# Performance work log

Measured on AMD Instinct MI355X. Metric: run time of the kernel, lower is better.

Reference implementation:

```python
import jax, jax.numpy as jnp
import numpy as np

B, T, E, H = 4, 1024, 1024, 16
F = E // H  # head_feature = 64
EPS = 1e-5


def setup_inputs() -> dict:
    key = jax.random.key(0)
    ks = jax.random.split(key, 7)
    return {
        "x": jax.random.normal(ks[0], (B, T, E), dtype=jnp.float32),
        "q_w": jax.random.normal(ks[1], (H, E, F), dtype=jnp.float32),
        "k_w": jax.random.normal(ks[2], (H, E, F), dtype=jnp.float32),
        "v_w": jax.random.normal(ks[3], (H, E, F), dtype=jnp.float32),
        "fr_w": jax.random.normal(ks[4], (B, E, E), dtype=jnp.float32),
        "ff_w": jax.random.normal(ks[5], (E, E), dtype=jnp.float32),
        "ff_b": jax.random.normal(ks[6], (E,), dtype=jnp.float32),
        "ln1_w": jnp.ones((T, E), dtype=jnp.float32),
        "ln1_b": jnp.zeros((T, E), dtype=jnp.float32),
        "ln2_w": jnp.ones((T, E), dtype=jnp.float32),
        "ln2_b": jnp.zeros((T, E), dtype=jnp.float32),
    }


def _layernorm_2d(x, w, b):
    # LayerNorm over the last TWO dims ([T, E]), matching nn.LayerNorm([T, E])
    mean = jnp.mean(x, axis=(-2, -1), keepdims=True)
    var = jnp.mean(jnp.square(x - mean), axis=(-2, -1), keepdims=True)
    return (x - mean) * jax.lax.rsqrt(var + EPS) * w + b


def _attention(x, q_w, k_w, v_w, fr_w):
    # projections: [B,T,E] x [H,E,F] -> [B,H,T,F]
    q = jnp.einsum("bte,hef->bhtf", x, q_w)
    k = jnp.einsum("bte,hef->bhtf", x, k_w)
    v = jnp.einsum("bte,hef->bhtf", x, v_w)
    scores = jnp.einsum("bhqf,bhkf->bhqk", q, k)  # [B,H,T,T]
    # faithful to source: multiplicative mask (-1e9 on strict upper tri, +1 added everywhere)
    ones = jnp.ones((T, T), dtype=scores.dtype)
    mask = -1.0e9 * jnp.triu(ones, k=1) + ones
    scores = scores * mask
    attn = jax.nn.softmax(scores / jnp.sqrt(jnp.float32(F)), axis=-1)
    z = jnp.einsum("bhqk,bhkf->bhqf", attn, v)  # [B,H,T,F]
    z = z.transpose(0, 2, 1, 3).reshape(B, T, E)  # merge heads
    return jnp.einsum("bte,bed->btd", z, fr_w)  # per-batch feature reduction


def reference(x, q_w, k_w, v_w, fr_w, ff_w, ff_b, ln1_w, ln1_b, ln2_w, ln2_b):
    z = _attention(x, q_w, k_w, v_w, fr_w)
    z1 = _layernorm_2d(x + z, ln1_w, ln1_b)
    z2 = jax.nn.relu(jnp.einsum("bte,de->btd", z1, ff_w) + ff_b)
    return _layernorm_2d(z1 + z2, ln2_w, ln2_b)
```

## Files before the change

kernel.cpp:

```cpp
#include <hip/hip_runtime.h>
#include <math.h>

constexpr int Bc = 4, Tc = 1024, Ec = 1024, Hc = 16, Fc = 64;

typedef __attribute__((ext_vector_type(8))) short bf16x8;
typedef __attribute__((ext_vector_type(4))) float f32x4;

__device__ __forceinline__ ushort f2bf(float x) {
  union { float f; unsigned u; } v; v.f = x;
  unsigned r = v.u + 0x7fffu + ((v.u >> 16) & 1u);
  return (ushort)(r >> 16);
}
__device__ __forceinline__ float bf2f(ushort h) {
  union { float f; unsigned u; } v; v.u = ((unsigned)h) << 16; return v.f;
}
__device__ __forceinline__ void split3(float x, ushort& h, ushort& m, ushort& l) {
  h = f2bf(x);
  float r1 = x - bf2f(h);
  m = f2bf(r1);
  float r2 = r1 - bf2f(m);
  l = f2bf(r2);
}
__device__ __forceinline__ void split2(float x, ushort& h, ushort& l) {
  h = f2bf(x);
  l = f2bf(x - bf2f(h));
}

__global__ __launch_bounds__(256) void transp_w(
    const float* __restrict__ qw, const float* __restrict__ kw,
    const float* __restrict__ vw, ushort* __restrict__ wT)
{
  const int zi = blockIdx.z;
  const float* src = (zi == 0) ? qw : (zi == 1) ? kw : vw;
  ushort* dst = wT + (size_t)(zi * 3) * (1u << 20);
  const int ns = (zi == 2) ? 1 : 3;
  const int h = blockIdx.y, e0 = blockIdx.x * 64;
  __shared__ float T[64][68];
  const int tid = threadIdx.x;
  {
    const int er = tid >> 4, fr = (tid & 15) * 4;
#pragma unroll
    for (int i = 0; i < 4; ++i) {
      const float4 v = *(const float4*)&src[((size_t)(h * 1024 + e0 + er + i * 16)) * 64 + fr];
      *(float4*)&T[er + i * 16][fr] = v;
    }
  }
  __syncthreads();
  const int f = tid >> 2, eo = (tid & 3) * 16;
  ushort hs[16], ms[16], ls[16];
#pragma unroll
  for (int j = 0; j < 16; ++j) {
    split3(T[eo + j][f], hs[j], ms[j], ls[j]);
  }
  const size_t nbase = (size_t)(h * 64 + f) * 1024 + e0 + eo;
  bf16x8 v0, v1;
#pragma unroll
  for (int j = 0; j < 8; ++j) { v0[j] = (short)hs[j]; v1[j] = (short)hs[j + 8]; }
  *(bf16x8*)&dst[nbase] = v0; *(bf16x8*)&dst[nbase + 8] = v1;
  if (ns == 3) {
#pragma unroll
    for (int j = 0; j < 8; ++j) { v0[j] = (short)ms[j]; v1[j] = (short)ms[j + 8]; }
    *(bf16x8*)&dst[(1u << 20) + nbase] = v0; *(bf16x8*)&dst[(1u << 20) + nbase + 8] = v1;
#pragma unroll
    for (int j = 0; j < 8; ++j) { v0[j] = (short)ls[j]; v1[j] = (short)ls[j + 8]; }
    *(bf16x8*)&dst[(2u << 20) + nbase] = v0; *(bf16x8*)&dst[(2u << 20) + nbase + 8] = v1;
  }
}

__global__ __launch_bounds__(256) void transp_frw(
    const float* __restrict__ frw, ushort* __restrict__ frT)
{
  const int bb = blockIdx.z;
  const int e0 = blockIdx.x * 64, d0 = blockIdx.y * 64;
  __shared__ float T[64][68];
  const int tid = threadIdx.x;
  {
    const int er = tid >> 4, dr = (tid & 15) * 4;
#pragma unroll
    for (int i = 0; i < 4; ++i) {
      const float4 v = *(const float4*)&frw[((size_t)bb * 1024 + e0 + er + i * 16) * 1024 + d0 + dr];
      *(float4*)&T[er + i * 16][dr] = v;
    }
  }
  __syncthreads();
  const int d = tid >> 2, eo = (tid & 3) * 16;
  ushort hs[16], ls[16];
#pragma unroll
  for (int j = 0; j < 16; ++j) split2(T[eo + j][d], hs[j], ls[j]);
  const size_t nbase = ((size_t)bb * 1024 + d0 + d) * 1024 + e0 + eo;
  bf16x8 v0, v1;
#pragma unroll
  for (int j = 0; j < 8; ++j) { v0[j] = (short)hs[j]; v1[j] = (short)hs[j + 8]; }
  *(bf16x8*)&frT[nbase] = v0; *(bf16x8*)&frT[nbase + 8] = v1;
#pragma unroll
  for (int j = 0; j < 8; ++j) { v0[j] = (short)ls[j]; v1[j] = (short)ls[j + 8]; }
  *(bf16x8*)&frT[(4u << 20) + nbase] = v0; *(bf16x8*)&frT[(4u << 20) + nbase + 8] = v1;
}

__global__ __launch_bounds__(256) void proj_qk_mfma(
    const float* __restrict__ x, const ushort* __restrict__ wT,
    float* __restrict__ qf, ushort* __restrict__ kh,
    ushort* __restrict__ km, ushort* __restrict__ kl)
{
  const int zi = blockIdx.z;
  const ushort* wt = wT + (size_t)zi * 3 * (1u << 20);
  const int m0 = blockIdx.x * 128, n0 = blockIdx.y * 128;
  __shared__ ushort As[3][128][36];
  __shared__ ushort Bs[3][128][36];
  const int tid = threadIdx.x;
  const int wave = tid >> 6, lane = tid & 63, l15 = lane & 15, quad = lane >> 4;
  const int wm = wave >> 1, wn = wave & 1;
  const int sr = tid >> 1, sk = (tid & 1) * 16;
  f32x4 acc[4][4] = {};
  for (int k0 = 0; k0 < 1024; k0 += 32) {
    __syncthreads();
    {
      const float* ap = x + (size_t)(m0 + sr) * 1024 + k0 + sk;
      float xs[16];
      *(float4*)&xs[0]  = *(const float4*)(ap);
      *(float4*)&xs[4]  = *(const float4*)(ap + 4);
      *(float4*)&xs[8]  = *(const float4*)(ap + 8);
      *(float4*)&xs[12] = *(const float4*)(ap + 12);
      bf16x8 h0, h1, m0v, m1v, l0, l1;
#pragma unroll
      for (int j = 0; j < 8; ++j) {
        ushort hu, mu, lu;
        split3(xs[j], hu, mu, lu);
        h0[j] = (short)hu; m0v[j] = (short)mu; l0[j] = (short)lu;
        split3(xs[j + 8], hu, mu, lu);
        h1[j] = (short)hu; m1v[j] = (short)mu; l1[j] = (short)lu;
      }
      *(bf16x8*)&As[0][sr][sk] = h0;  *(bf16x8*)&As[0][sr][sk + 8] = h1;
      *(bf16x8*)&As[1][sr][sk] = m0v; *(bf16x8*)&As[1][sr][sk + 8] = m1v;
      *(bf16x8*)&As[2][sr][sk] = l0;  *(bf16x8*)&As[2][sr][sk + 8] = l1;
#pragma unroll
      for (int s = 0; s < 3; ++s) {
        const ushort* bp = wt + ((size_t)s << 20) + (size_t)(n0 + sr) * 1024 + k0 + sk;
        *(bf16x8*)&Bs[s][sr][sk]     = *(const bf16x8*)(bp);
        *(bf16x8*)&Bs[s][sr][sk + 8] = *(const bf16x8*)(bp + 8);
      }
    }
    __syncthreads();
    bf16x8 af[4][3];
#pragma unroll
    for (int tm = 0; tm < 4; ++tm)
#pragma unroll
      for (int s = 0; s < 3; ++s)
        af[tm][s] = *(const bf16x8*)&As[s][wm * 64 + tm * 16 + l15][quad * 8];
#pragma unroll
    for (int tn = 0; tn < 4; ++tn) {
      const int nrow = wn * 64 + tn * 16 + l15;
      bf16x8 b0 = *(const bf16x8*)&Bs[0][nrow][quad * 8];
      bf16x8 b1 = *(const bf16x8*)&Bs[1][nrow][quad * 8];
      bf16x8 b2 = *(const bf16x8*)&Bs[2][nrow][quad * 8];
#pragma unroll
      for (int tm = 0; tm < 4; ++tm) {
        f32x4 a = acc[tm][tn];
        a = __builtin_amdgcn_mfma_f32_16x16x32_bf16(af[tm][0], b0, a, 0, 0, 0);
        a = __builtin_amdgcn_mfma_f32_16x16x32_bf16(af[tm][0], b1, a, 0, 0, 0);
        a = __builtin_amdgcn_mfma_f32_16x16x32_bf16(af[tm][1], b0, a, 0, 0, 0);
        a = __builtin_amdgcn_mfma_f32_16x16x32_bf16(af[tm][0], b2, a, 0, 0, 0);
        a = __builtin_amdgcn_mfma_f32_16x16x32_bf16(af[tm][1], b1, a, 0, 0, 0);
        a = __builtin_amdgcn_mfma_f32_16x16x32_bf16(af[tm][2], b0, a, 0, 0, 0);
        acc[tm][tn] = a;
      }
    }
  }
#pragma unroll
  for (int tm = 0; tm < 4; ++tm) {
#pragma unroll
    for (int tn = 0; tn < 4; ++tn) {
#pragma unroll
      for (int r = 0; r < 4; ++r) {
        int m = m0 + wm * 64 + tm * 16 + quad * 4 + r;
        int n = n0 + wn * 64 + tn * 16 + l15;
        int b = m >> 10, t = m & 1023, h = n >> 6, f = n & 63;
        size_t idx = (((size_t)(b * 16 + h)) * 1024 + t) * 64 + f;
        if (zi == 0) {
          qf[idx] = acc[tm][tn][r];
        } else {
          ushort hu, mu, lu;
          split3(acc[tm][tn][r], hu, mu, lu);
          kh[idx] = hu; km[idx] = mu; kl[idx] = lu;
        }
      }
    }
  }
}

__global__ __launch_bounds__(256) void proj_v_mfma(
    const float* __restrict__ x, const ushort* __restrict__ wT,
    ushort* __restrict__ vt)
{
  const ushort* wt = wT + (size_t)6 * (1u << 20);
  const int m0 = blockIdx.x * 128, n0 = blockIdx.y * 128;
  __shared__ ushort As[128][36];
  __shared__ ushort Bs[128][36];
  const int tid = threadIdx.x;
  const int wave = tid >> 6, lane = tid & 63, l15 = lane & 15, quad = lane >> 4;
  const int wm = wave >> 1, wn = wave & 1;
  const int sr = tid >> 1, sk = (tid & 1) * 16;
  f32x4 acc[4][4] = {};
  for (int k0 = 0; k0 < 1024; k0 += 32) {
    __syncthreads();
    {
      const float* ap = x + (size_t)(m0 + sr) * 1024 + k0 + sk;
      float xs[16];
      *(float4*)&xs[0]  = *(const float4*)(ap);
      *(float4*)&xs[4]  = *(const float4*)(ap + 4);
      *(float4*)&xs[8]  = *(const float4*)(ap + 8);
      *(float4*)&xs[12] = *(const float4*)(ap + 12);
      bf16x8 h0, h1;
#pragma unroll
      for (int j = 0; j < 8; ++j) {
        h0[j] = (short)f2bf(xs[j]);
        h1[j] = (short)f2bf(xs[j + 8]);
      }
      *(bf16x8*)&As[sr][sk] = h0; *(bf16x8*)&As[sr][sk + 8] = h1;
      const ushort* bp = wt + (size_t)(n0 + sr) * 1024 + k0 + sk;
      *(bf16x8*)&Bs[sr][sk]     = *(const bf16x8*)(bp);
      *(bf16x8*)&Bs[sr][sk + 8] = *(const bf16x8*)(bp + 8);
    }
    __syncthreads();
    bf16x8 af[4];
#pragma unroll
    for (int tm = 0; tm < 4; ++tm)
      af[tm] = *(const bf16x8*)&As[wm * 64 + tm * 16 + l15][quad * 8];
#pragma unroll
    for (int tn = 0; tn < 4; ++tn) {
      bf16x8 b0 = *(const bf16x8*)&Bs[wn * 64 + tn * 16 + l15][quad * 8];
#pragma unroll
      for (int tm = 0; tm < 4; ++tm)
        acc[tm][tn] = __builtin_amdgcn_mfma_f32_16x16x32_bf16(af[tm], b0, acc[tm][tn], 0, 0, 0);
    }
  }
#pragma unroll
  for (int tm = 0; tm < 4; ++tm) {
#pragma unroll
    for (int tn = 0; tn < 4; ++tn) {
#pragma unroll
      for (int r = 0; r < 4; ++r) {
        int m = m0 + wm * 64 + tm * 16 + quad * 4 + r;
        int n = n0 + wn * 64 + tn * 16 + l15;
        int b = m >> 10, t = m & 1023, h = n >> 6, f = n & 63;
        vt[(((size_t)(b * 16 + h)) * 64 + f) * 1024 + t] = f2bf(acc[tm][tn][r]);
      }
    }
  }
}

__global__ __launch_bounds__(512) void attn_mfma(
    const float* __restrict__ qf, const ushort* __restrict__ kh,
    const ushort* __restrict__ km, const ushort* __restrict__ kl,
    const ushort* __restrict__ vt, float* __restrict__ z)
{
  __shared__ ushort Ks[3][64][68];
  __shared__ ushort Vs[64][68];
  __shared__ ushort Pl[8][16][68];

  const int tid = threadIdx.x;
  const int wave = tid >> 6, lane = tid & 63;
  const int l15 = lane & 15, quad = lane >> 4;
  const int bh = blockIdx.y;
  const int qbase = blockIdx.x * 128;

  bf16x8 aqh[2], aqm[2], aql[2];
  {
    const int qrow = qbase + wave * 16 + l15;
    const float* qp = qf + ((size_t)bh * Tc + qrow) * Fc;
#pragma unroll
    for (int ks = 0; ks < 2; ++ks) {
      int f0 = ks * 32 + quad * 8;
      float4 x0 = *(const float4*)(qp + f0);
      float4 x1 = *(const float4*)(qp + f0 + 4);
      float xs[8] = {x0.x, x0.y, x0.z, x0.w, x1.x, x1.y, x1.z, x1.w};
#pragma unroll
      for (int j = 0; j < 8; ++j) {
        ushort hu, mu, lu;
        split3(xs[j], hu, mu, lu);
        aqh[ks][j] = (short)hu; aqm[ks][j] = (short)mu; aql[ks][j] = (short)lu;
      }
    }
  }

  f32x4 o[4] = {{0,0,0,0},{0,0,0,0},{0,0,0,0},{0,0,0,0}};
  float m_run[4], l_run[4];
#pragma unroll
  for (int r = 0; r < 4; ++r) { m_run[r] = -1e30f; l_run[r] = 0.f; }

  const int srow = tid >> 3, sc8 = tid & 7;
  const size_t kbase = (size_t)bh * Tc * Fc;
  const size_t vbase = (size_t)bh * Fc * Tc;
  const ushort* kp0 = kh + kbase + (size_t)srow * Fc + sc8 * 8;
  const ushort* kp1 = km + kbase + (size_t)srow * Fc + sc8 * 8;
  const ushort* kp2 = kl + kbase + (size_t)srow * Fc + sc8 * 8;
  const ushort* vp  = vt + vbase + (size_t)srow * Tc + sc8 * 8;

  for (int kt = 0; kt < Tc; kt += 64) {
    __syncthreads();
    {
      const size_t ko = (size_t)kt * Fc;
      *(bf16x8*)&Ks[0][srow][sc8 * 8] = *(const bf16x8*)(kp0 + ko);
      *(bf16x8*)&Ks[1][srow][sc8 * 8] = *(const bf16x8*)(kp1 + ko);
      *(bf16x8*)&Ks[2][srow][sc8 * 8] = *(const bf16x8*)(kp2 + ko);
      *(bf16x8*)&Vs[srow][sc8 * 8]    = *(const bf16x8*)(vp + kt);
    }
    __syncthreads();

    f32x4 sacc[4] = {{0,0,0,0},{0,0,0,0},{0,0,0,0},{0,0,0,0}};
#pragma unroll
    for (int nt = 0; nt < 4; ++nt) {
      int key = nt * 16 + l15;
#pragma unroll
      for (int ks = 0; ks < 2; ++ks) {
        int f0 = ks * 32 + quad * 8;
        bf16x8 bh_ = *(const bf16x8*)&Ks[0][key][f0];
        bf16x8 bm_ = *(const bf16x8*)&Ks[1][key][f0];
        bf16x8 bl_ = *(const bf16x8*)&Ks[2][key][f0];
        sacc[nt] = __builtin_amdgcn_mfma_f32_16x16x32_bf16(aqh[ks], bh_, sacc[nt], 0, 0, 0);
        sacc[nt] = __builtin_amdgcn_mfma_f32_16x16x32_bf16(aqh[ks], bm_, sacc[nt], 0, 0, 0);
        sacc[nt] = __builtin_amdgcn_mfma_f32_16x16x32_bf16(aqm[ks], bh_, sacc[nt], 0, 0, 0);
        sacc[nt] = __builtin_amdgcn_mfma_f32_16x16x32_bf16(aqh[ks], bl_, sacc[nt], 0, 0, 0);
        sacc[nt] = __builtin_amdgcn_mfma_f32_16x16x32_bf16(aqm[ks], bm_, sacc[nt], 0, 0, 0);
        sacc[nt] = __builtin_amdgcn_mfma_f32_16x16x32_bf16(aql[ks], bh_, sacc[nt], 0, 0, 0);
      }
    }

    const int rowg0 = qbase + wave * 16 + quad * 4;
    float mx[4];
#pragma unroll
    for (int r = 0; r < 4; ++r) mx[r] = -1e30f;
#pragma unroll
    for (int nt = 0; nt < 4; ++nt) {
      int key = kt + nt * 16 + l15;
#pragma unroll
      for (int r = 0; r < 4; ++r) {
        float s = sacc[nt][r];
        if (key > rowg0 + r) s *= -1.0e9f + 1.0f;
        s *= 0.125f;
        sacc[nt][r] = s;
        mx[r] = fmaxf(mx[r], s);
      }
    }
#pragma unroll
    for (int r = 0; r < 4; ++r)
#pragma unroll
      for (int d = 1; d < 16; d <<= 1) mx[r] = fmaxf(mx[r], __shfl_xor(mx[r], d));

    float corr[4], ps[4];
#pragma unroll
    for (int r = 0; r < 4; ++r) {
      float m2 = fmaxf(m_run[r], mx[r]);
      corr[r] = __expf(m_run[r] - m2);
      m_run[r] = m2;
      ps[r] = 0.f;
    }
#pragma unroll
    for (int nt = 0; nt < 4; ++nt) {
#pragma unroll
      for (int r = 0; r < 4; ++r) {
        float p = __expf(sacc[nt][r] - m_run[r]);
        ps[r] += p;
        Pl[wave][quad * 4 + r][nt * 16 + l15] = f2bf(p);
      }
    }
#pragma unroll
    for (int r = 0; r < 4; ++r) {
#pragma unroll
      for (int d = 1; d < 16; d <<= 1) ps[r] += __shfl_xor(ps[r], d);
      l_run[r] = l_run[r] * corr[r] + ps[r];
#pragma unroll
      for (int ft = 0; ft < 4; ++ft) o[ft][r] *= corr[r];
    }

#pragma unroll
    for (int ks2 = 0; ks2 < 2; ++ks2) {
      bf16x8 pa = *(const bf16x8*)&Pl[wave][l15][ks2 * 32 + quad * 8];
#pragma unroll
      for (int ft = 0; ft < 4; ++ft) {
        bf16x8 vb = *(const bf16x8*)&Vs[ft * 16 + l15][ks2 * 32 + quad * 8];
        o[ft] = __builtin_amdgcn_mfma_f32_16x16x32_bf16(pa, vb, o[ft], 0, 0, 0);
      }
    }
  }

  const int b = bh >> 4, h = bh & 15;
#pragma unroll
  for (int r = 0; r < 4; ++r) {
    float inv = 1.f / l_run[r];
    int row = qbase + wave * 16 + quad * 4 + r;
    float* zp = z + ((size_t)(b * Tc + row)) * Ec + h * Fc;
#pragma unroll
    for (int ft = 0; ft < 4; ++ft) zp[ft * 16 + l15] = o[ft][r] * inv;
  }
}

__global__ __launch_bounds__(256) void gemm_fr_mfma(
    const float* __restrict__ z, const ushort* __restrict__ frT,
    const float* __restrict__ x, float* __restrict__ s1,
    float2* __restrict__ part)
{
  const int bb = blockIdx.z;
  const int m0 = blockIdx.x * 128, n0 = blockIdx.y * 128;
  __shared__ ushort Ah[128][36], Al[128][36];
  __shared__ ushort Bh[128][36], Bl[128][36];
  __shared__ float2 red[256];
  const int tid = threadIdx.x;
  const int wave = tid >> 6, lane = tid & 63, l15 = lane & 15, quad = lane >> 4;
  const int wm = wave >> 1, wn = wave & 1;
  const int sr = tid >> 1, sk = (tid & 1) * 16;
  f32x4 acc[4][4] = {};
  const ushort* bhp = frT + ((size_t)bb * 1024 + n0) * 1024;
  const ushort* blp = bhp + (4u << 20);
  for (int k0 = 0; k0 < 1024; k0 += 32) {
    __syncthreads();
    {
      const float* ap = z + ((size_t)bb * 1024 + m0 + sr) * 1024 + k0 + sk;
      float xs[16];
      *(float4*)&xs[0]  = *(const float4*)(ap);
      *(float4*)&xs[4]  = *(const float4*)(ap + 4);
      *(float4*)&xs[8]  = *(const float4*)(ap + 8);
      *(float4*)&xs[12] = *(const float4*)(ap + 12);
      bf16x8 h0, h1, l0, l1;
#pragma unroll
      for (int j = 0; j < 8; ++j) {
        ushort hu, lu;
        split2(xs[j], hu, lu);     h0[j] = (short)hu; l0[j] = (short)lu;
        split2(xs[j + 8], hu, lu); h1[j] = (short)hu; l1[j] = (short)lu;
      }
      *(bf16x8*)&Ah[sr][sk] = h0; *(bf16x8*)&Ah[sr][sk + 8] = h1;
      *(bf16x8*)&Al[sr][sk] = l0; *(bf16x8*)&Al[sr][sk + 8] = l1;
      const size_t boff = (size_t)sr * 1024 + k0 + sk;
      *(bf16x8*)&Bh[sr][sk]     = *(const bf16x8*)(bhp + boff);
      *(bf16x8*)&Bh[sr][sk + 8] = *(const bf16x8*)(bhp + boff + 8);
      *(bf16x8*)&Bl[sr][sk]     = *(const bf16x8*)(blp + boff);
      *(bf16x8*)&Bl[sr][sk + 8] = *(const bf16x8*)(blp + boff + 8);
    }
    __syncthreads();
    bf16x8 ah[4], al[4];
#pragma unroll
    for (int tm = 0; tm < 4; ++tm) {
      ah[tm] = *(const bf16x8*)&Ah[wm * 64 + tm * 16 + l15][quad * 8];
      al[tm] = *(const bf16x8*)&Al[wm * 64 + tm * 16 + l15][quad * 8];
    }
#pragma unroll
    for (int tn = 0; tn < 4; ++tn) {
      const int nrow = wn * 64 + tn * 16 + l15;
      bf16x8 b0 = *(const bf16x8*)&Bh[nrow][quad * 8];
      bf16x8 b1 = *(const bf16x8*)&Bl[nrow][quad * 8];
#pragma unroll
      for (int tm = 0; tm < 4; ++tm) {
        f32x4 a = acc[tm][tn];
        a = __builtin_amdgcn_mfma_f32_16x16x32_bf16(ah[tm], b0, a, 0, 0, 0);
        a = __builtin_amdgcn_mfma_f32_16x16x32_bf16(ah[tm], b1, a, 0, 0, 0);
        a = __builtin_amdgcn_mfma_f32_16x16x32_bf16(al[tm], b0, a, 0, 0, 0);
        acc[tm][tn] = a;
      }
    }
  }
  float sum = 0.f, sq = 0.f;
#pragma unroll
  for (int tm = 0; tm < 4; ++tm) {
#pragma unroll
    for (int tn = 0; tn < 4; ++tn) {
#pragma unroll
      for (int r = 0; r < 4; ++r) {
        int m = m0 + wm * 64 + tm * 16 + quad * 4 + r;
        int n = n0 + wn * 64 + tn * 16 + l15;
        size_t idx = ((size_t)bb * 1024 + m) * 1024 + n;
        float o = x[idx] + acc[tm][tn][r];
        s1[idx] = o;
        sum += o; sq += o * o;
      }
    }
  }
  red[tid] = make_float2(sum, sq);
  __syncthreads();
  for (int s = 128; s > 0; s >>= 1) {
    if (tid < s) { red[tid].x += red[tid + s].x; red[tid].y += red[tid + s].y; }
    __syncthreads();
  }
  if (tid == 0) part[(bb * 8 + blockIdx.x) * 8 + blockIdx.y] = red[0];
}

__global__ __launch_bounds__(256) void gemm_ff_mfma(
    const float* __restrict__ z1, const float* __restrict__ ffw,
    const float* __restrict__ ffb, float* __restrict__ s2,
    float2* __restrict__ part)
{
  const int m0 = blockIdx.x * 128, n0 = blockIdx.y * 128;
  __shared__ ushort Ah[128][36], Al[128][36];
  __shared__ ushort Bh[128][36], Bl[128][36];
  __shared__ float2 red[256];
  const int tid = threadIdx.x;
  const int wave = tid >> 6, lane = tid & 63, l15 = lane & 15, quad = lane >> 4;
  const int wm = wave >> 1, wn = wave & 1;
  const int sr = tid >> 1, sk = (tid & 1) * 16;
  f32x4 acc[4][4] = {};
  for (int k0 = 0; k0 < 1024; k0 += 32) {
    __syncthreads();
    {
      const float* ap = z1 + (size_t)(m0 + sr) * 1024 + k0 + sk;
      const float* bp = ffw + (size_t)(n0 + sr) * 1024 + k0 + sk;
      float xs[16], ys[16];
      *(float4*)&xs[0]  = *(const float4*)(ap);
      *(float4*)&xs[4]  = *(const float4*)(ap + 4);
      *(float4*)&xs[8]  = *(const float4*)(ap + 8);
      *(float4*)&xs[12] = *(const float4*)(ap + 12);
      *(float4*)&ys[0]  = *(const float4*)(bp);
      *(float4*)&ys[4]  = *(const float4*)(bp + 4);
      *(float4*)&ys[8]  = *(const float4*)(bp + 8);
      *(float4*)&ys[12] = *(const float4*)(bp + 12);
      bf16x8 h0, h1, l0, l1, g0, g1, e0, e1;
#pragma unroll
      for (int j = 0; j < 8; ++j) {
        ushort hu, lu;
        split2(xs[j], hu, lu);     h0[j] = (short)hu; l0[j] = (short)lu;
        split2(xs[j + 8], hu, lu); h1[j] = (short)hu; l1[j] = (short)lu;
        split2(ys[j], hu, lu);     g0[j] = (short)hu; e0[j] = (short)lu;
        split2(ys[j + 8], hu, lu); g1[j] = (short)hu; e1[j] = (short)lu;
      }
      *(bf16x8*)&Ah[sr][sk] = h0; *(bf16x8*)&Ah[sr][sk + 8] = h1;
      *(bf16x8*)&Al[sr][sk] = l0; *(bf16x8*)&Al[sr][sk + 8] = l1;
      *(bf16x8*)&Bh[sr][sk] = g0; *(bf16x8*)&Bh[sr][sk + 8] = g1;
      *(bf16x8*)&Bl[sr][sk] = e0; *(bf16x8*)&Bl[sr][sk + 8] = e1;
    }
    __syncthreads();
    bf16x8 ah[4], al[4];
#pragma unroll
    for (int tm = 0; tm < 4; ++tm) {
      ah[tm] = *(const bf16x8*)&Ah[wm * 64 + tm * 16 + l15][quad * 8];
      al[tm] = *(const bf16x8*)&Al[wm * 64 + tm * 16 + l15][quad * 8];
    }
#pragma unroll
    for (int tn = 0; tn < 4; ++tn) {
      const int nrow = wn * 64 + tn * 16 + l15;
      bf16x8 b0 = *(const bf16x8*)&Bh[nrow][quad * 8];
      bf16x8 b1 = *(const bf16x8*)&Bl[nrow][quad * 8];
#pragma unroll
      for (int tm = 0; tm < 4; ++tm) {
        f32x4 a = acc[tm][tn];
        a = __builtin_amdgcn_mfma_f32_16x16x32_bf16(ah[tm], b0, a, 0, 0, 0);
        a = __builtin_amdgcn_mfma_f32_16x16x32_bf16(ah[tm], b1, a, 0, 0, 0);
        a = __builtin_amdgcn_mfma_f32_16x16x32_bf16(al[tm], b0, a, 0, 0, 0);
        acc[tm][tn] = a;
      }
    }
  }
  float sum = 0.f, sq = 0.f;
#pragma unroll
  for (int tm = 0; tm < 4; ++tm) {
#pragma unroll
    for (int tn = 0; tn < 4; ++tn) {
#pragma unroll
      for (int r = 0; r < 4; ++r) {
        int m = m0 + wm * 64 + tm * 16 + quad * 4 + r;
        int n = n0 + wn * 64 + tn * 16 + l15;
        size_t idx = (size_t)m * 1024 + n;
        float o = z1[idx] + fmaxf(acc[tm][tn][r] + ffb[n], 0.f);
        s2[idx] = o;
        sum += o; sq += o * o;
      }
    }
  }
  red[tid] = make_float2(sum, sq);
  __syncthreads();
  for (int s = 128; s > 0; s >>= 1) {
    if (tid < s) { red[tid].x += red[tid + s].x; red[tid].y += red[tid + s].y; }
    __syncthreads();
  }
  if (tid == 0) part[blockIdx.x * 8 + blockIdx.y] = red[0];
}

__global__ __launch_bounds__(256) void ln_stats(
    const float2* __restrict__ part, float2* __restrict__ stats, int npart)
{
  __shared__ double sd[256], sq[256];
  const int tid = threadIdx.x;
  float2 p = (tid < npart) ? part[blockIdx.x * npart + tid] : make_float2(0.f, 0.f);
  sd[tid] = (double)p.x; sq[tid] = (double)p.y;
  __syncthreads();
  for (int s = 128; s > 0; s >>= 1) {
    if (tid < s) { sd[tid] += sd[tid + s]; sq[tid] += sq[tid + s]; }
    __syncthreads();
  }
  if (tid == 0) {
    const double n = (double)Tc * Ec;
    double mean = sd[0] / n;
    double var = sq[0] / n - mean * mean;
    if (var < 0.0) var = 0.0;
    double rs = 1.0 / sqrt(var + 1e-5);
    stats[blockIdx.x] = make_float2((float)mean, (float)rs);
  }
}

__global__ __launch_bounds__(256) void ln_norm(
    const float* __restrict__ s, const float2* __restrict__ stats,
    const float* __restrict__ w, const float* __restrict__ bias,
    float* __restrict__ out)
{
  int i = blockIdx.x * 256 + threadIdx.x;
  if (i >= (Bc * Tc * Ec) / 4) return;
  int b = i >> 18;
  int te4 = i & ((1 << 18) - 1);
  float2 st = stats[b];
  float4 sv = ((const float4*)s)[i];
  float4 wv = ((const float4*)w)[te4];
  float4 bv = ((const float4*)bias)[te4];
  float4 o;
  o.x = (sv.x - st.x) * st.y * wv.x + bv.x;
  o.y = (sv.y - st.x) * st.y * wv.y + bv.y;
  o.z = (sv.z - st.x) * st.y * wv.z + bv.z;
  o.w = (sv.w - st.x) * st.y * wv.w + bv.w;
  ((float4*)out)[i] = o;
}

extern "C" void kernel_launch(void* const* d_in, const int* in_sizes, int n_in,
                              void* d_out, int out_size, void* d_ws, size_t ws_size,
                              hipStream_t stream)
{
  const float* x    = (const float*)d_in[0];
  const float* qw   = (const float*)d_in[1];
  const float* kw   = (const float*)d_in[2];
  const float* vw   = (const float*)d_in[3];
  const float* frw  = (const float*)d_in[4];
  const float* ffw  = (const float*)d_in[5];
  const float* ffb  = (const float*)d_in[6];
  const float* ln1w = (const float*)d_in[7];
  const float* ln1b = (const float*)d_in[8];
  const float* ln2w = (const float*)d_in[9];
  const float* ln2b = (const float*)d_in[10];
  float* out = (float*)d_out;
  char* W = (char*)d_ws;

  const size_t MB = 1ull << 20;
  float*  qf  = (float*)(W);
  ushort* kh  = (ushort*)(W + 16 * MB);
  ushort* km  = (ushort*)(W + 24 * MB);
  ushort* kl  = (ushort*)(W + 32 * MB);
  ushort* vt  = (ushort*)(W + 40 * MB);
  ushort* wT  = (ushort*)(W + 48 * MB);
  float*  zb  = (float*)(W + 48 * MB);
  ushort* frT = (ushort*)(W + 16 * MB);
  float*  s1  = (float*)(W);
  float*  z1  = (float*)(W + 16 * MB);
  float*  s2  = (float*)(W + 32 * MB);
  float2* part1  = (float2*)(W + 64 * MB);
  float2* part2  = part1 + 1024;
  float2* stats1 = part2 + 1024;
  float2* stats2 = stats1 + 4;

  transp_w<<<dim3(16, 16, 3), 256, 0, stream>>>(qw, kw, vw, wT);
  proj_qk_mfma<<<dim3(32, 8, 2), 256, 0, stream>>>(x, wT, qf, kh, km, kl);
  proj_v_mfma<<<dim3(32, 8), 256, 0, stream>>>(x, wT, vt);
  attn_mfma<<<dim3(8, 64), 512, 0, stream>>>(qf, kh, km, kl, vt, zb);
  transp_frw<<<dim3(16, 16, 4), 256, 0, stream>>>(frw, frT);
  gemm_fr_mfma<<<dim3(8, 8, 4), 256, 0, stream>>>(zb, frT, x, s1, part1);
  ln_stats<<<dim3(4), 256, 0, stream>>>(part1, stats1, 64);
  ln_norm<<<dim3(4096), 256, 0, stream>>>(s1, stats1, ln1w, ln1b, z1);
  gemm_ff_mfma<<<dim3(32, 8), 256, 0, stream>>>(z1, ffw, ffb, s2, part2);
  ln_stats<<<dim3(4), 256, 0, stream>>>(part2, stats2, 64);
  ln_norm<<<dim3(4096), 256, 0, stream>>>(s2, stats2, ln2w, ln2b, out);
}
```

Baseline: 480.7 us.

## Pre-split GEMM operands to bf16 and use fragment-ordered LDS layout

Moves the fp32-to-bf16 hi/lo splitting out of the GEMM inner loops. The attention epilogue, layernorm-1 and a new split_ffw kernel now emit split bf16 buffers, so gemm_fr and gemm_ff only copy bf16 tiles into LDS. The LDS tiles are reorganized into an MFMA-fragment-contiguous layout without padding to avoid bank conflicts. The QK projection switches to a truncating 3-way split, which changes rounding but keeps the residual exact. This adds an extra kernel launch and keeps padding-free LDS strides, which may create conflicts on the store side.

```diff
diff --git a/kernel.cpp b/kernel.cpp
--- a/kernel.cpp
+++ b/kernel.cpp
@@ -25,6 +25,20 @@
   h = f2bf(x);
   l = f2bf(x - bf2f(h));
 }
+__device__ __forceinline__ void split3t(float x, ushort& h, ushort& m, ushort& l) {
+  union { float f; unsigned u; } v; v.f = x;
+  h = (ushort)(v.u >> 16);
+  union { float f; unsigned u; } hf; hf.u = v.u & 0xffff0000u;
+  float r1 = x - hf.f;
+  union { float f; unsigned u; } v1; v1.f = r1;
+  m = (ushort)(v1.u >> 16);
+  union { float f; unsigned u; } mf; mf.u = v1.u & 0xffff0000u;
+  float r2 = r1 - mf.f;
+  union { float f; unsigned u; } v2; v2.f = r2;
+  l = (ushort)(v2.u >> 16);
+}
+
+#define FRAG_IDX(tile, quad, l) (((((tile) * 4) + (quad)) * 16 + (l)) * 8)
 
 __global__ __launch_bounds__(256) void transp_w(
     const float* __restrict__ qw, const float* __restrict__ kw,
@@ -49,9 +63,7 @@
   const int f = tid >> 2, eo = (tid & 3) * 16;
   ushort hs[16], ms[16], ls[16];
 #pragma unroll
-  for (int j = 0; j < 16; ++j) {
-    split3(T[eo + j][f], hs[j], ms[j], ls[j]);
-  }
+  for (int j = 0; j < 16; ++j) split3(T[eo + j][f], hs[j], ms[j], ls[j]);
   const size_t nbase = (size_t)(h * 64 + f) * 1024 + e0 + eo;
   bf16x8 v0, v1;
 #pragma unroll
@@ -97,6 +109,17 @@
   *(bf16x8*)&frT[(4u << 20) + nbase] = v0; *(bf16x8*)&frT[(4u << 20) + nbase + 8] = v1;
 }
 
+__global__ __launch_bounds__(256) void split_ffw(
+    const float* __restrict__ ffw, ushort* __restrict__ fh, ushort* __restrict__ fl)
+{
+  int i = blockIdx.x * 256 + threadIdx.x;
+  float4 v = ((const float4*)ffw)[i];
+  ushort4 h, l;
+  split2(v.x, h.x, l.x); split2(v.y, h.y, l.y);
+  split2(v.z, h.z, l.z); split2(v.w, h.w, l.w);
+  ((ushort4*)fh)[i] = h; ((ushort4*)fl)[i] = l;
+}
+
 __global__ __launch_bounds__(256) void proj_qk_mfma(
     const float* __restrict__ x, const ushort* __restrict__ wT,
     float* __restrict__ qf, ushort* __restrict__ kh,
@@ -105,17 +128,19 @@
   const int zi = blockIdx.z;
   const ushort* wt = wT + (size_t)zi * 3 * (1u << 20);
   const int m0 = blockIdx.x * 128, n0 = blockIdx.y * 128;
-  __shared__ ushort As[3][128][36];
-  __shared__ ushort Bs[3][128][36];
+  __shared__ ushort As[3 * 4096];
+  __shared__ ushort Bs[3 * 4096];
   const int tid = threadIdx.x;
   const int wave = tid >> 6, lane = tid & 63, l15 = lane & 15, quad = lane >> 4;
   const int wm = wave >> 1, wn = wave & 1;
-  const int sr = tid >> 1, sk = (tid & 1) * 16;
+  const int sr = tid >> 1, q0 = (tid & 1) * 2;
+  const int wb0 = FRAG_IDX(sr >> 4, q0, sr & 15);
+  const int wb1 = FRAG_IDX(sr >> 4, q0 + 1, sr & 15);
   f32x4 acc[4][4] = {};
   for (int k0 = 0; k0 < 1024; k0 += 32) {
     __syncthreads();
     {
-      const float* ap = x + (size_t)(m0 + sr) * 1024 + k0 + sk;
+      const float* ap = x + (size_t)(m0 + sr) * 1024 + k0 + q0 * 8;
       float xs[16];
       *(float4*)&xs[0]  = *(const float4*)(ap);
       *(float4*)&xs[4]  = *(const float4*)(ap + 4);
@@ -125,19 +150,19 @@
 #pragma unroll
       for (int j = 0; j < 8; ++j) {
         ushort hu, mu, lu;
-        split3(xs[j], hu, mu, lu);
+        split3t(xs[j], hu, mu, lu);
         h0[j] = (short)hu; m0v[j] = (short)mu; l0[j] = (short)lu;
-        split3(xs[j + 8], hu, mu, lu);
+        split3t(xs[j + 8], hu, mu, lu);
         h1[j] = (short)hu; m1v[j] = (short)mu; l1[j] = (short)lu;
       }
-      *(bf16x8*)&As[0][sr][sk] = h0;  *(bf16x8*)&As[0][sr][sk + 8] = h1;
-      *(bf16x8*)&As[1][sr][sk] = m0v; *(bf16x8*)&As[1][sr][sk + 8] = m1v;
-      *(bf16x8*)&As[2][sr][sk] = l0;  *(bf16x8*)&As[2][sr][sk + 8] = l1;
+      *(bf16x8*)&As[wb0] = h0;          *(bf16x8*)&As[wb1] = h1;
+      *(bf16x8*)&As[4096 + wb0] = m0v;  *(bf16x8*)&As[4096 + wb1] = m1v;
+      *(bf16x8*)&As[8192 + wb0] = l0;   *(bf16x8*)&As[8192 + wb1] = l1;
 #pragma unroll
       for (int s = 0; s < 3; ++s) {
-        const ushort* bp = wt + ((size_t)s << 20) + (size_t)(n0 + sr) * 1024 + k0 + sk;
-        *(bf16x8*)&Bs[s][sr][sk]     = *(const bf16x8*)(bp);
-        *(bf16x8*)&Bs[s][sr][sk + 8] = *(const bf16x8*)(bp + 8);
+        const ushort* bp = wt + ((size_t)s << 20) + (size_t)(n0 + sr) * 1024 + k0 + q0 * 8;
+        *(bf16x8*)&Bs[s * 4096 + wb0] = *(const bf16x8*)(bp);
+        *(bf16x8*)&Bs[s * 4096 + wb1] = *(const bf16x8*)(bp + 8);
       }
     }
     __syncthreads();
@@ -146,13 +171,13 @@
     for (int tm = 0; tm < 4; ++tm)
 #pragma unroll
       for (int s = 0; s < 3; ++s)
-        af[tm][s] = *(const bf16x8*)&As[s][wm * 64 + tm * 16 + l15][quad * 8];
+        af[tm][s] = *(const bf16x8*)&As[s * 4096 + FRAG_IDX(wm * 4 + tm, quad, l15)];
 #pragma unroll
     for (int tn = 0; tn < 4; ++tn) {
-      const int nrow = wn * 64 + tn * 16 + l15;
-      bf16x8 b0 = *(const bf16x8*)&Bs[0][nrow][quad * 8];
-      bf16x8 b1 = *(const bf16x8*)&Bs[1][nrow][quad * 8];
-      bf16x8 b2 = *(const bf16x8*)&Bs[2][nrow][quad * 8];
+      const int bi = FRAG_IDX(wn * 4 + tn, quad, l15);
+      bf16x8 b0 = *(const bf16x8*)&Bs[bi];
+      bf16x8 b1 = *(const bf16x8*)&Bs[4096 + bi];
+      bf16x8 b2 = *(const bf16x8*)&Bs[8192 + bi];
 #pragma unroll
       for (int tm = 0; tm < 4; ++tm) {
         f32x4 a = acc[tm][tn];
@@ -194,17 +219,19 @@
 {
   const ushort* wt = wT + (size_t)6 * (1u << 20);
   const int m0 = blockIdx.x * 128, n0 = blockIdx.y * 128;
-  __shared__ ushort As[128][36];
-  __shared__ ushort Bs[128][36];
+  __shared__ ushort As[4096];
+  __shared__ ushort Bs[4096];
   const int tid = threadIdx.x;
   const int wave = tid >> 6, lane = tid & 63, l15 = lane & 15, quad = lane >> 4;
   const int wm = wave >> 1, wn = wave & 1;
-  const int sr = tid >> 1, sk = (tid & 1) * 16;
+  const int sr = tid >> 1, q0 = (tid & 1) * 2;
+  const int wb0 = FRAG_IDX(sr >> 4, q0, sr & 15);
+  const int wb1 = FRAG_IDX(sr >> 4, q0 + 1, sr & 15);
   f32x4 acc[4][4] = {};
   for (int k0 = 0; k0 < 1024; k0 += 32) {
     __syncthreads();
     {
-      const float* ap = x + (size_t)(m0 + sr) * 1024 + k0 + sk;
+      const float* ap = x + (size_t)(m0 + sr) * 1024 + k0 + q0 * 8;
       float xs[16];
       *(float4*)&xs[0]  = *(const float4*)(ap);
       *(float4*)&xs[4]  = *(const float4*)(ap + 4);
@@ -216,19 +243,19 @@
         h0[j] = (short)f2bf(xs[j]);
         h1[j] = (short)f2bf(xs[j + 8]);
       }
-      *(bf16x8*)&As[sr][sk] = h0; *(bf16x8*)&As[sr][sk + 8] = h1;
-      const ushort* bp = wt + (size_t)(n0 + sr) * 1024 + k0 + sk;
-      *(bf16x8*)&Bs[sr][sk]     = *(const bf16x8*)(bp);
-      *(bf16x8*)&Bs[sr][sk + 8] = *(const bf16x8*)(bp + 8);
+      *(bf16x8*)&As[wb0] = h0; *(bf16x8*)&As[wb1] = h1;
+      const ushort* bp = wt + (size_t)(n0 + sr) * 1024 + k0 + q0 * 8;
+      *(bf16x8*)&Bs[wb0] = *(const bf16x8*)(bp);
+      *(bf16x8*)&Bs[wb1] = *(const bf16x8*)(bp + 8);
     }
     __syncthreads();
     bf16x8 af[4];
 #pragma unroll
     for (int tm = 0; tm < 4; ++tm)
-      af[tm] = *(const bf16x8*)&As[wm * 64 + tm * 16 + l15][quad * 8];
+      af[tm] = *(const bf16x8*)&As[FRAG_IDX(wm * 4 + tm, quad, l15)];
 #pragma unroll
     for (int tn = 0; tn < 4; ++tn) {
-      bf16x8 b0 = *(const bf16x8*)&Bs[wn * 64 + tn * 16 + l15][quad * 8];
+      bf16x8 b0 = *(const bf16x8*)&Bs[FRAG_IDX(wn * 4 + tn, quad, l15)];
 #pragma unroll
       for (int tm = 0; tm < 4; ++tm)
         acc[tm][tn] = __builtin_amdgcn_mfma_f32_16x16x32_bf16(af[tm], b0, acc[tm][tn], 0, 0, 0);
@@ -252,7 +279,7 @@
 __global__ __launch_bounds__(512) void attn_mfma(
     const float* __restrict__ qf, const ushort* __restrict__ kh,
     const ushort* __restrict__ km, const ushort* __restrict__ kl,
-    const ushort* __restrict__ vt, float* __restrict__ z)
+    const ushort* __restrict__ vt, ushort* __restrict__ zh, ushort* __restrict__ zl)
 {
   __shared__ ushort Ks[3][64][68];
   __shared__ ushort Vs[64][68];
@@ -389,65 +416,60 @@
   for (int r = 0; r < 4; ++r) {
     float inv = 1.f / l_run[r];
     int row = qbase + wave * 16 + quad * 4 + r;
-    float* zp = z + ((size_t)(b * Tc + row)) * Ec + h * Fc;
-#pragma unroll
-    for (int ft = 0; ft < 4; ++ft) zp[ft * 16 + l15] = o[ft][r] * inv;
+    size_t base = ((size_t)(b * Tc + row)) * Ec + h * Fc;
+#pragma unroll
+    for (int ft = 0; ft < 4; ++ft) {
+      ushort hu, lu;
+      split2(o[ft][r] * inv, hu, lu);
+      zh[base + ft * 16 + l15] = hu;
+      zl[base + ft * 16 + l15] = lu;
+    }
   }
 }
 
 __global__ __launch_bounds__(256) void gemm_fr_mfma(
-    const float* __restrict__ z, const ushort* __restrict__ frT,
-    const float* __restrict__ x, float* __restrict__ s1,
-    float2* __restrict__ part)
+    const ushort* __restrict__ zh, const ushort* __restrict__ zl,
+    const ushort* __restrict__ frT, const float* __restrict__ x,
+    float* __restrict__ s1, float2* __restrict__ part)
 {
   const int bb = blockIdx.z;
   const int m0 = blockIdx.x * 128, n0 = blockIdx.y * 128;
-  __shared__ ushort Ah[128][36], Al[128][36];
-  __shared__ ushort Bh[128][36], Bl[128][36];
+  __shared__ ushort Ah[4096], Al[4096], Bh[4096], Bl[4096];
   __shared__ float2 red[256];
   const int tid = threadIdx.x;
   const int wave = tid >> 6, lane = tid & 63, l15 = lane & 15, quad = lane >> 4;
   const int wm = wave >> 1, wn = wave & 1;
-  const int sr = tid >> 1, sk = (tid & 1) * 16;
+  const int sr = tid >> 1, q0 = (tid & 1) * 2;
+  const int wb0 = FRAG_IDX(sr >> 4, q0, sr & 15);
+  const int wb1 = FRAG_IDX(sr >> 4, q0 + 1, sr & 15);
   f32x4 acc[4][4] = {};
-  const ushort* bhp = frT + ((size_t)bb * 1024 + n0) * 1024;
-  const ushort* blp = bhp + (4u << 20);
+  const size_t abase = ((size_t)bb * 1024 + m0 + sr) * 1024 + q0 * 8;
+  const size_t bbase = ((size_t)bb * 1024 + n0 + sr) * 1024 + q0 * 8;
+  const ushort* blp = frT + (4u << 20);
   for (int k0 = 0; k0 < 1024; k0 += 32) {
     __syncthreads();
     {
-      const float* ap = z + ((size_t)bb * 1024 + m0 + sr) * 1024 + k0 + sk;
-      float xs[16];
-      *(float4*)&xs[0]  = *(const float4*)(ap);
-      *(float4*)&xs[4]  = *(const float4*)(ap + 4);
-      *(float4*)&xs[8]  = *(const float4*)(ap + 8);
-      *(float4*)&xs[12] = *(const float4*)(ap + 12);
-      bf16x8 h0, h1, l0, l1;
-#pragma unroll
-      for (int j = 0; j < 8; ++j) {
-        ushort hu, lu;
-        split2(xs[j], hu, lu);     h0[j] = (short)hu; l0[j] = (short)lu;
-        split2(xs[j + 8], hu, lu); h1[j] = (short)hu; l1[j] = (short)lu;
-      }
-      *(bf16x8*)&Ah[sr][sk] = h0; *(bf16x8*)&Ah[sr][sk + 8] = h1;
-      *(bf16x8*)&Al[sr][sk] = l0; *(bf16x8*)&Al[sr][sk + 8] = l1;
-      const size_t boff = (size_t)sr * 1024 + k0 + sk;
-      *(bf16x8*)&Bh[sr][sk]     = *(const bf16x8*)(bhp + boff);
-      *(bf16x8*)&Bh[sr][sk + 8] = *(const bf16x8*)(bhp + boff + 8);
-      *(bf16x8*)&Bl[sr][sk]     = *(const bf16x8*)(blp + boff);
-      *(bf16x8*)&Bl[sr][sk + 8] = *(const bf16x8*)(blp + boff + 8);
+      *(bf16x8*)&Ah[wb0] = *(const bf16x8*)(zh + abase + k0);
+      *(bf16x8*)&Ah[wb1] = *(const bf16x8*)(zh + abase + k0 + 8);
+      *(bf16x8*)&Al[wb0] = *(const bf16x8*)(zl + abase + k0);
+      *(bf16x8*)&Al[wb1] = *(const bf16x8*)(zl + abase + k0 + 8);
+      *(bf16x8*)&Bh[wb0] = *(const bf16x8*)(frT + bbase + k0);
+      *(bf16x8*)&Bh[wb1] = *(const bf16x8*)(frT + bbase + k0 + 8);
+      *(bf16x8*)&Bl[wb0] = *(const bf16x8*)(blp + bbase + k0);
+      *(bf16x8*)&Bl[wb1] = *(const bf16x8*)(blp + bbase + k0 + 8);
     }
     __syncthreads();
     bf16x8 ah[4], al[4];
 #pragma unroll
     for (int tm = 0; tm < 4; ++tm) {
-      ah[tm] = *(const bf16x8*)&Ah[wm * 64 + tm * 16 + l15][quad * 8];
-      al[tm] = *(const bf16x8*)&Al[wm * 64 + tm * 16 + l15][quad * 8];
+      ah[tm] = *(const bf16x8*)&Ah[FRAG_IDX(wm * 4 + tm, quad, l15)];
+      al[tm] = *(const bf16x8*)&Al[FRAG_IDX(wm * 4 + tm, quad, l15)];
     }
 #pragma unroll
     for (int tn = 0; tn < 4; ++tn) {
-      const int nrow = wn * 64 + tn * 16 + l15;
-      bf16x8 b0 = *(const bf16x8*)&Bh[nrow][quad * 8];
-      bf16x8 b1 = *(const bf16x8*)&Bl[nrow][quad * 8];
+      const int bi = FRAG_IDX(wn * 4 + tn, quad, l15);
+      bf16x8 b0 = *(const bf16x8*)&Bh[bi];
+      bf16x8 b1 = *(const bf16x8*)&Bl[bi];
 #pragma unroll
       for (int tm = 0; tm < 4; ++tm) {
         f32x4 a = acc[tm][tn];
@@ -484,59 +506,47 @@
 }
 
 __global__ __launch_bounds__(256) void gemm_ff_mfma(
-    const float* __restrict__ z1, const float* __restrict__ ffw,
+    const ushort* __restrict__ z1h, const ushort* __restrict__ z1l,
+    const ushort* __restrict__ fwh, const ushort* __restrict__ fwl,
     const float* __restrict__ ffb, float* __restrict__ s2,
     float2* __restrict__ part)
 {
   const int m0 = blockIdx.x * 128, n0 = blockIdx.y * 128;
-  __shared__ ushort Ah[128][36], Al[128][36];
-  __shared__ ushort Bh[128][36], Bl[128][36];
+  __shared__ ushort Ah[4096], Al[4096], Bh[4096], Bl[4096];
   __shared__ float2 red[256];
   const int tid = threadIdx.x;
   const int wave = tid >> 6, lane = tid & 63, l15 = lane & 15, quad = lane >> 4;
   const int wm = wave >> 1, wn = wave & 1;
-  const int sr = tid >> 1, sk = (tid & 1) * 16;
+  const int sr = tid >> 1, q0 = (tid & 1) * 2;
+  const int wb0 = FRAG_IDX(sr >> 4, q0, sr & 15);
+  const int wb1 = FRAG_IDX(sr >> 4, q0 + 1, sr & 15);
   f32x4 acc[4][4] = {};
+  const size_t abase = (size_t)(m0 + sr) * 1024 + q0 * 8;
+  const size_t bbase = (size_t)(n0 + sr) * 1024 + q0 * 8;
   for (int k0 = 0; k0 < 1024; k0 += 32) {
     __syncthreads();
     {
-      const float* ap = z1 + (size_t)(m0 + sr) * 1024 + k0 + sk;
-      const float* bp = ffw + (size_t)(n0 + sr) * 1024 + k0 + sk;
-      float xs[16], ys[16];
-      *(float4*)&xs[0]  = *(const float4*)(ap);
-      *(float4*)&xs[4]  = *(const float4*)(ap + 4);
-      *(float4*)&xs[8]  = *(const float4*)(ap + 8);
-      *(float4*)&xs[12] = *(const float4*)(ap + 12);
-      *(float4*)&ys[0]  = *(const float4*)(bp);
-      *(float4*)&ys[4]  = *(const float4*)(bp + 4);
-      *(float4*)&ys[8]  = *(const float4*)(bp + 8);
-      *(float4*)&ys[12] = *(const float4*)(bp + 12);
-      bf16x8 h0, h1, l0, l1, g0, g1, e0, e1;
-#pragma unroll
-      for (int j = 0; j < 8; ++j) {
-        ushort hu, lu;
-        split2(xs[j], hu, lu);     h0[j] = (short)hu; l0[j] = (short)lu;
-        split2(xs[j + 8], hu, lu); h1[j] = (short)hu; l1[j] = (short)lu;
-        split2(ys[j], hu, lu);     g0[j] = (short)hu; e0[j] = (short)lu;
-        split2(ys[j + 8], hu, lu); g1[j] = (short)hu; e1[j] = (short)lu;
-      }
-      *(bf16x8*)&Ah[sr][sk] = h0; *(bf16x8*)&Ah[sr][sk + 8] = h1;
-      *(bf16x8*)&Al[sr][sk] = l0; *(bf16x8*)&Al[sr][sk + 8] = l1;
-      *(bf16x8*)&Bh[sr][sk] = g0; *(bf16x8*)&Bh[sr][sk + 8] = g1;
-      *(bf16x8*)&Bl[sr][sk] = e0; *(bf16x8*)&Bl[sr][sk + 8] = e1;
+      *(bf16x8*)&Ah[wb0] = *(const bf16x8*)(z1h + abase + k0);
+      *(bf16x8*)&Ah[wb1] = *(const bf16x8*)(z1h + abase + k0 + 8);
+      *(bf16x8*)&Al[wb0] = *(const bf16x8*)(z1l + abase + k0);
+      *(bf16x8*)&Al[wb1] = *(const bf16x8*)(z1l + abase + k0 + 8);
+      *(bf16x8*)&Bh[wb0] = *(const bf16x8*)(fwh + bbase + k0);
+      *(bf16x8*)&Bh[wb1] = *(const bf16x8*)(fwh + bbase + k0 + 8);
+      *(bf16x8*)&Bl[wb0] = *(const bf16x8*)(fwl + bbase + k0);
+      *(bf16x8*)&Bl[wb1] = *(const bf16x8*)(fwl + bbase + k0 + 8);
     }
     __syncthreads();
     bf16x8 ah[4], al[4];
 #pragma unroll
     for (int tm = 0; tm < 4; ++tm) {
-      ah[tm] = *(const bf16x8*)&Ah[wm * 64 + tm * 16 + l15][quad * 8];
-      al[tm] = *(const bf16x8*)&Al[wm * 64 + tm * 16 + l15][quad * 8];
+      ah[tm] = *(const bf16x8*)&Ah[FRAG_IDX(wm * 4 + tm, quad, l15)];
+      al[tm] = *(const bf16x8*)&Al[FRAG_IDX(wm * 4 + tm, quad, l15)];
     }
 #pragma unroll
     for (int tn = 0; tn < 4; ++tn) {
-      const int nrow = wn * 64 + tn * 16 + l15;
-      bf16x8 b0 = *(const bf16x8*)&Bh[nrow][quad * 8];
-      bf16x8 b1 = *(const bf16x8*)&Bl[nrow][quad * 8];
+      const int bi = FRAG_IDX(wn * 4 + tn, quad, l15);
+      bf16x8 b0 = *(const bf16x8*)&Bh[bi];
+      bf16x8 b1 = *(const bf16x8*)&Bl[bi];
 #pragma unroll
       for (int tm = 0; tm < 4; ++tm) {
         f32x4 a = acc[tm][tn];
@@ -557,7 +567,8 @@
         int m = m0 + wm * 64 + tm * 16 + quad * 4 + r;
         int n = n0 + wn * 64 + tn * 16 + l15;
         size_t idx = (size_t)m * 1024 + n;
-        float o = z1[idx] + fmaxf(acc[tm][tn][r] + ffb[n], 0.f);
+        float z1v = bf2f(z1h[idx]) + bf2f(z1l[idx]);
+        float o = z1v + fmaxf(acc[tm][tn][r] + ffb[n], 0.f);
         s2[idx] = o;
         sum += o; sq += o * o;
       }
@@ -592,6 +603,30 @@
     double rs = 1.0 / sqrt(var + 1e-5);
     stats[blockIdx.x] = make_float2((float)mean, (float)rs);
   }
+}
+
+__global__ __launch_bounds__(256) void ln_norm_split(
+    const float* __restrict__ s, const float2* __restrict__ stats,
+    const float* __restrict__ w, const float* __restrict__ bias,
+    ushort* __restrict__ oh, ushort* __restrict__ ol)
+{
+  int i = blockIdx.x * 256 + threadIdx.x;
+  if (i >= (Bc * Tc * Ec) / 4) return;
+  int b = i >> 18;
+  int te4 = i & ((1 << 18) - 1);
+  float2 st = stats[b];
+  float4 sv = ((const float4*)s)[i];
+  float4 wv = ((const float4*)w)[te4];
+  float4 bv = ((const float4*)bias)[te4];
+  float4 o;
+  o.x = (sv.x - st.x) * st.y * wv.x + bv.x;
+  o.y = (sv.y - st.x) * st.y * wv.y + bv.y;
+  o.z = (sv.z - st.x) * st.y * wv.z + bv.z;
+  o.w = (sv.w - st.x) * st.y * wv.w + bv.w;
+  ushort4 h, l;
+  split2(o.x, h.x, l.x); split2(o.y, h.y, l.y);
+  split2(o.z, h.z, l.z); split2(o.w, h.w, l.w);
+  ((ushort4*)oh)[i] = h; ((ushort4*)ol)[i] = l;
 }
 
 __global__ __launch_bounds__(256) void ln_norm(
@@ -640,10 +675,14 @@
   ushort* kl  = (ushort*)(W + 32 * MB);
   ushort* vt  = (ushort*)(W + 40 * MB);
   ushort* wT  = (ushort*)(W + 48 * MB);
-  float*  zb  = (float*)(W + 48 * MB);
+  ushort* zh  = (ushort*)(W + 48 * MB);
+  ushort* zl  = (ushort*)(W + 56 * MB);
   ushort* frT = (ushort*)(W + 16 * MB);
   float*  s1  = (float*)(W);
-  float*  z1  = (float*)(W + 16 * MB);
+  ushort* z1h = (ushort*)(W + 16 * MB);
+  ushort* z1l = (ushort*)(W + 24 * MB);
+  ushort* fwh = (ushort*)(W + 48 * MB);
+  ushort* fwl = (ushort*)(W + 50 * MB);
   float*  s2  = (float*)(W + 32 * MB);
   float2* part1  = (float2*)(W + 64 * MB);
   float2* part2  = part1 + 1024;
@@ -653,12 +692,13 @@
   transp_w<<<dim3(16, 16, 3), 256, 0, stream>>>(qw, kw, vw, wT);
   proj_qk_mfma<<<dim3(32, 8, 2), 256, 0, stream>>>(x, wT, qf, kh, km, kl);
   proj_v_mfma<<<dim3(32, 8), 256, 0, stream>>>(x, wT, vt);
-  attn_mfma<<<dim3(8, 64), 512, 0, stream>>>(qf, kh, km, kl, vt, zb);
+  attn_mfma<<<dim3(8, 64), 512, 0, stream>>>(qf, kh, km, kl, vt, zh, zl);
   transp_frw<<<dim3(16, 16, 4), 256, 0, stream>>>(frw, frT);
-  gemm_fr_mfma<<<dim3(8, 8, 4), 256, 0, stream>>>(zb, frT, x, s1, part1);
+  gemm_fr_mfma<<<dim3(8, 8, 4), 256, 0, stream>>>(zh, zl, frT, x, s1, part1);
   ln_stats<<<dim3(4), 256, 0, stream>>>(part1, stats1, 64);
-  ln_norm<<<dim3(4096), 256, 0, stream>>>(s1, stats1, ln1w, ln1b, z1);
-  gemm_ff_mfma<<<dim3(32, 8), 256, 0, stream>>>(z1, ffw, ffb, s2, part2);
+  ln_norm_split<<<dim3(4096), 256, 0, stream>>>(s1, stats1, ln1w, ln1b, z1h, z1l);
+  split_ffw<<<dim3(1024), 256, 0, stream>>>(ffw, fwh, fwl);
+  gemm_ff_mfma<<<dim3(32, 8), 256, 0, stream>>>(z1h, z1l, fwh, fwl, ffb, s2, part2);
   ln_stats<<<dim3(4), 256, 0, stream>>>(part2, stats2, 64);
   ln_norm<<<dim3(4096), 256, 0, stream>>>(s2, stats2, ln2w, ln2b, out);
 }
```

After: 446.5 us. -7.1%, faster.
